# Performance work log

Hardware: AMD Instinct MI355X
Metric: run time of the kernel (lower is better)

## Reference

```python
import jax, jax.numpy as jnp
import numpy as np

N = 100000   # total nodes across all graphs
E = 200000   # directed edges
B = 128      # number of graphs in the batch
IN1, IN2 = 128, 128
IN = IN1 + IN2      # in_feats = 256 (x || x_da)
HID = 64
OUT = 64


def setup_inputs() -> dict:
    key = jax.random.key(0)
    ks = jax.random.split(key, 6)
    x = jax.random.normal(ks[0], (N, IN1), jnp.float32)
    x_da = jax.random.normal(ks[1], (N, IN2), jnp.float32)
    edge_index = jax.random.randint(ks[2], (2, E), 0, N, dtype=jnp.int32)
    # equal, sorted, non-empty segments (graph ids) -- mirrors sorted PyG batch vector
    batch = (jnp.arange(N, dtype=jnp.int32) * B) // N
    # root node of graph b = first node of its segment
    rootindex = (jnp.arange(B, dtype=jnp.int32) * N) // B
    s1 = 1.0 / np.sqrt(IN)
    W1 = jax.random.uniform(ks[3], (IN, HID), jnp.float32, -s1, s1)
    b1 = jnp.zeros((HID,), jnp.float32)
    s2 = 1.0 / np.sqrt(HID + IN)
    W2 = jax.random.uniform(ks[4], (HID + IN, OUT), jnp.float32, -s2, s2)
    b2 = jnp.zeros((OUT,), jnp.float32)
    return dict(x=x, x_da=x_da, edge_index=edge_index, batch=batch,
                rootindex=rootindex, W1=W1, b1=b1, W2=W2, b2=b2)


def gcn_conv(x, edge_index, W, b):
    """PyG GCNConv: symmetric-normalized A+I message passing after a linear."""
    n = x.shape[0]
    h = x @ W                                   # [n, out] linear first (as in PyG)
    src, dst = edge_index[0], edge_index[1]
    # degree on target nodes, +1 for the added self loop
    deg = jnp.zeros((n,), h.dtype).at[dst].add(jnp.ones((src.shape[0],), h.dtype)) + 1.0
    dinv = jax.lax.rsqrt(deg)
    norm = dinv[src] * dinv[dst]                # [E]
    agg = jnp.zeros_like(h).at[dst].add(h[src] * norm[:, None])
    agg = agg + h * (dinv * dinv)[:, None]      # self-loop term: 1/deg
    return agg + b


def reference(x, x_da, edge_index, batch, rootindex, W1, b1, W2, b2):
    x0 = jnp.concatenate([x, x_da], axis=1)     # [N, IN]
    x1 = x0                                     # saved original features
    h = gcn_conv(x0, edge_index, W1, b1)        # [N, HID]
    x2 = h                                      # saved conv1 output
    # vectorized root-feature broadcast: replaces the python per-graph loop
    root1 = x1[rootindex[batch]]                # [N, IN]
    h = jax.nn.relu(jnp.concatenate([h, root1], axis=1))  # [N, HID+IN]
    # F.dropout with training=False is identity (eval mode)
    h = gcn_conv(h, edge_index, W2, b2)         # [N, OUT]
    h = jax.nn.relu(h)
    root2 = x2[rootindex[batch]]                # [N, HID]
    h = jnp.concatenate([h, root2], axis=1)     # [N, OUT+HID]
    # scatter_mean over graph ids
    sums = jax.ops.segment_sum(h, batch, num_segments=B)
    counts = jax.ops.segment_sum(jnp.ones((h.shape[0], 1), h.dtype), batch, num_segments=B)
    return sums / counts                        # [B, OUT+HID]
```

## Files before the change

### kernel.cpp

```cpp
#include <hip/hip_runtime.h>

#define IN1 128
#define K1 256
#define HID 64
#define MCH 16

typedef __attribute__((ext_vector_type(8))) __bf16 bf16x8;
typedef __attribute__((ext_vector_type(4))) __bf16 bf16x4;
typedef __attribute__((ext_vector_type(8))) unsigned short u16x8;
typedef __attribute__((ext_vector_type(4))) float f32x4;

__device__ __forceinline__ int swz(int row, int k, int ldk) {
    return (row * ldk + k) ^ ((row & 7) << 3);
}

__global__ __launch_bounds__(256) void count_edges(const int* __restrict__ ei, int* counts, int E) {
    int e = blockIdx.x * 256 + threadIdx.x;
    if (e < E) atomicAdd(&counts[ei[E + e]], 1);
}

__global__ __launch_bounds__(256) void block_sums_dinv(const int* __restrict__ counts,
                                                       int* __restrict__ bsum,
                                                       float* __restrict__ dinv, int N) {
    __shared__ int sh[256];
    int i = blockIdx.x * 256 + threadIdx.x;
    int v = (i < N) ? counts[i] : 0;
    if (i < N) dinv[i] = rsqrtf((float)v + 1.0f);
    sh[threadIdx.x] = v;
    __syncthreads();
    for (int off = 128; off > 0; off >>= 1) {
        if (threadIdx.x < off) sh[threadIdx.x] += sh[threadIdx.x + off];
        __syncthreads();
    }
    if (threadIdx.x == 0) bsum[blockIdx.x] = sh[0];
}

__global__ __launch_bounds__(512) void scan_and_segs(const int* __restrict__ bsum,
                                                     int* __restrict__ boff, int nb,
                                                     const int* __restrict__ batch,
                                                     int* __restrict__ segs, int N, int B) {
    if (blockIdx.x == 0) {
        __shared__ int sh[512];
        int t = threadIdx.x;
        int v = (t < nb) ? bsum[t] : 0;
        sh[t] = v;
        __syncthreads();
        for (int off = 1; off < 512; off <<= 1) {
            int u = (t >= off) ? sh[t - off] : 0;
            __syncthreads();
            sh[t] += u;
            __syncthreads();
        }
        if (t < nb) boff[t] = sh[t] - v;
    } else {
        int b = threadIdx.x;
        if (b > B) return;
        if (b == B) { segs[B] = N; return; }
        int lo = 0, hi = N;
        while (lo < hi) {
            int mid = (lo + hi) >> 1;
            if (batch[mid] < b) lo = mid + 1; else hi = mid;
        }
        segs[b] = lo;
    }
}

__global__ __launch_bounds__(256) void write_rowstart(const int* __restrict__ counts,
                                                      const int* __restrict__ boff,
                                                      int* __restrict__ rowstart, int N, int E) {
    __shared__ int sh[256];
    int i = blockIdx.x * 256 + threadIdx.x;
    int t = threadIdx.x;
    int v = (i < N) ? counts[i] : 0;
    sh[t] = v;
    __syncthreads();
    for (int off = 1; off < 256; off <<= 1) {
        int u = (t >= off) ? sh[t - off] : 0;
        __syncthreads();
        sh[t] += u;
        __syncthreads();
    }
    if (i < N) rowstart[i] = boff[blockIdx.x] + sh[t] - v;
    if (i == 0) rowstart[N] = E;
}

__global__ __launch_bounds__(256) void scatter_csr(const int* __restrict__ ei,
                                                   const int* __restrict__ rowstart,
                                                   const float* __restrict__ dinv,
                                                   int* counts,
                                                   int* __restrict__ csr_src,
                                                   float* __restrict__ csr_w, int E) {
    int e = blockIdx.x * 256 + threadIdx.x;
    if (e >= E) return;
    int s = ei[e], d = ei[E + e];
    int pos = rowstart[d] + atomicSub(&counts[d], 1) - 1;
    csr_src[pos] = s;
    csr_w[pos] = dinv[s];
}

__global__ __launch_bounds__(256) void prep_w(const float* __restrict__ W1,
                                              const float* __restrict__ W2,
                                              __bf16* __restrict__ w1img,
                                              __bf16* __restrict__ w2img) {
    int tid = blockIdx.x * 256 + threadIdx.x;
    if (tid < 64 * K1) {
        int k = tid >> 6, n = tid & 63;
        w1img[swz(n, k, K1)] = (__bf16)W1[tid];
    } else if (tid < 64 * K1 + 64 * 64) {
        int e = tid - 64 * K1;
        int k = e >> 6, n = e & 63;
        w2img[swz(n, k, 64)] = (__bf16)W2[e];
    }
}

__global__ __launch_bounds__(256, 4) void gemm1_mfma(const float* __restrict__ x,
                                                     const float* __restrict__ xda,
                                                     const __bf16* __restrict__ w1img,
                                                     __bf16* __restrict__ h1, int N) {
    __shared__ __bf16 Ws[64 * K1];
    int tid = threadIdx.x;
#pragma unroll
    for (int i = 0; i < 8; ++i)
        reinterpret_cast<bf16x8*>(Ws)[i * 256 + tid] =
            reinterpret_cast<const bf16x8*>(w1img)[i * 256 + tid];
    __syncthreads();

    int w = tid >> 6, l = tid & 63;
    int lr = l & 15, lg = l >> 4;
    int arow = blockIdx.x * 64 + w * 16 + lr;
    int carow = min(arow, N - 1);
    const float4* px = reinterpret_cast<const float4*>(x + (size_t)carow * IN1) + lg * 2;
    const float4* pd = reinterpret_cast<const float4*>(xda + (size_t)carow * IN1) + lg * 2;

    f32x4 acc[4] = {};
    float4 buf[4][2];

#pragma unroll
    for (int t = 0; t < 4; ++t) {
        const float4* p = (t < 4) ? (px + t * 8) : (pd + (t - 4) * 8);
        buf[t][0] = p[0];
        buf[t][1] = p[1];
    }
#pragma unroll
    for (int t = 0; t < 8; ++t) {
        float4 fa = buf[t & 3][0], fb = buf[t & 3][1];
        if (t + 4 < 8) {
            int tn = t + 4;
            const float4* p = (tn < 4) ? (px + tn * 8) : (pd + (tn - 4) * 8);
            buf[t & 3][0] = p[0];
            buf[t & 3][1] = p[1];
        }
        bf16x8 af;
        af[0] = (__bf16)fa.x; af[1] = (__bf16)fa.y;
        af[2] = (__bf16)fa.z; af[3] = (__bf16)fa.w;
        af[4] = (__bf16)fb.x; af[5] = (__bf16)fb.y;
        af[6] = (__bf16)fb.z; af[7] = (__bf16)fb.w;
        int k0 = t * 32 + lg * 8;
#pragma unroll
        for (int c = 0; c < 4; ++c) {
            bf16x8 bfr = *reinterpret_cast<const bf16x8*>(&Ws[swz(c * 16 + lr, k0, K1)]);
            acc[c] = __builtin_amdgcn_mfma_f32_16x16x32_bf16(af, bfr, acc[c], 0, 0, 0);
        }
    }
#pragma unroll
    for (int c = 0; c < 4; ++c)
#pragma unroll
        for (int r = 0; r < 4; ++r) {
            int row = blockIdx.x * 64 + w * 16 + lg * 4 + r;
            if (row < N) h1[(size_t)row * HID + c * 16 + lr] = (__bf16)acc[c][r];
        }
}

__global__ __launch_bounds__(256, 4) void gemm2_mfma(const __bf16* __restrict__ x2,
                                                     const __bf16* __restrict__ w2img,
                                                     const float* __restrict__ rb2,
                                                     const int* __restrict__ batch,
                                                     __bf16* __restrict__ h2, int N) {
    __shared__ __bf16 Ws[64 * 64];
    int tid = threadIdx.x;
#pragma unroll
    for (int i = 0; i < 2; ++i)
        reinterpret_cast<bf16x8*>(Ws)[i * 256 + tid] =
            reinterpret_cast<const bf16x8*>(w2img)[i * 256 + tid];
    __syncthreads();

    int w = tid >> 6, l = tid & 63;
    int lr = l & 15, lg = l >> 4;
    int arow = blockIdx.x * 64 + w * 16 + lr;
    int carow = min(arow, N - 1);
    const u16x8* pa = reinterpret_cast<const u16x8*>(x2 + (size_t)carow * HID + lg * 8);

    u16x8 raw0 = pa[0];
    u16x8 raw1 = pa[2];
    f32x4 acc[4] = {};
#pragma unroll
    for (int t = 0; t < 2; ++t) {
        u16x8 raw = t ? raw1 : raw0;
        u16x8 rel;
#pragma unroll
        for (int i = 0; i < 8; ++i)
            rel[i] = (raw[i] & 0x8000) ? (unsigned short)0 : raw[i];
        bf16x8 af = *reinterpret_cast<bf16x8*>(&rel);
        int k0 = t * 32 + lg * 8;
#pragma unroll
        for (int c = 0; c < 4; ++c) {
            bf16x8 bfr = *reinterpret_cast<const bf16x8*>(&Ws[swz(c * 16 + lr, k0, 64)]);
            acc[c] = __builtin_amdgcn_mfma_f32_16x16x32_bf16(af, bfr, acc[c], 0, 0, 0);
        }
    }
#pragma unroll
    for (int r = 0; r < 4; ++r) {
        int row = blockIdx.x * 64 + w * 16 + lg * 4 + r;
        if (row >= N) continue;
        int b = batch[row];
        const float* rv = rb2 + (size_t)b * HID;
#pragma unroll
        for (int c = 0; c < 4; ++c)
            h2[(size_t)row * HID + c * 16 + lr] = (__bf16)(acc[c][r] + rv[c * 16 + lr]);
    }
}

__global__ __launch_bounds__(256) void gather(const int* __restrict__ rowstart,
                                              const int* __restrict__ csr_src,
                                              const float* __restrict__ csr_w,
                                              const __bf16* __restrict__ h,
                                              const float* __restrict__ dinv,
                                              const float* __restrict__ bias,
                                              __bf16* __restrict__ out, int N) {
    int t = blockIdx.x * 256 + threadIdx.x;
    int i = t >> 4, c = t & 15;
    if (i >= N) return;
    float di = dinv[i];
    float s2 = di * di;
    bf16x4 hv = *reinterpret_cast<const bf16x4*>(h + (size_t)i * HID + c * 4);
    float4 bv = reinterpret_cast<const float4*>(bias)[c];
    float a0 = fmaf((float)hv[0], s2, bv.x);
    float a1 = fmaf((float)hv[1], s2, bv.y);
    float a2 = fmaf((float)hv[2], s2, bv.z);
    float a3 = fmaf((float)hv[3], s2, bv.w);
    int k0 = rowstart[i], k1 = rowstart[i + 1];
    for (int k = k0; k < k1; ++k) {
        int s = csr_src[k];
        float wgt = csr_w[k] * di;
        bf16x4 sv = *reinterpret_cast<const bf16x4*>(h + (size_t)s * HID + c * 4);
        a0 = fmaf((float)sv[0], wgt, a0);
        a1 = fmaf((float)sv[1], wgt, a1);
        a2 = fmaf((float)sv[2], wgt, a2);
        a3 = fmaf((float)sv[3], wgt, a3);
    }
    bf16x4 o;
    o[0] = (__bf16)a0; o[1] = (__bf16)a1; o[2] = (__bf16)a2; o[3] = (__bf16)a3;
    *reinterpret_cast<bf16x4*>(out + (size_t)i * HID + c * 4) = o;
}

__global__ __launch_bounds__(64) void rb2_k(const float* __restrict__ x,
                                            const float* __restrict__ xda,
                                            const int* __restrict__ rootindex,
                                            const float* __restrict__ W2,
                                            float* __restrict__ rb2) {
    int b = blockIdx.x;
    int j = threadIdx.x;
    int root = rootindex[b];
    const float* xr = x + (size_t)root * IN1;
    const float* dr = xda + (size_t)root * IN1;
    float acc = 0.f;
    for (int k = 0; k < IN1; ++k) {
        float v = fmaxf(xr[k], 0.f);
        acc = fmaf(v, W2[(size_t)(HID + k) * HID + j], acc);
    }
    for (int k = 0; k < IN1; ++k) {
        float v = fmaxf(dr[k], 0.f);
        acc = fmaf(v, W2[(size_t)(HID + IN1 + k) * HID + j], acc);
    }
    rb2[b * HID + j] = acc;
}

__global__ __launch_bounds__(256) void mean_part(const __bf16* __restrict__ agg2,
                                                 const int* __restrict__ segs,
                                                 float* __restrict__ part) {
    int b = blockIdx.x / MCH, c = blockIdx.x % MCH;
    int s = segs[b], e = segs[b + 1];
    long len = e - s;
    int cs = s + (int)(len * c / MCH);
    int ce = s + (int)(len * (c + 1) / MCH);
    int f = threadIdx.x & 63, g = threadIdx.x >> 6;
    float p = 0.f;
    for (int i = cs + g; i < ce; i += 4)
        p += fmaxf((float)agg2[(size_t)i * HID + f], 0.f);
    __shared__ float red[4][64];
    red[g][f] = p;
    __syncthreads();
    if (g == 0)
        part[((size_t)b * MCH + c) * 64 + f] = red[0][f] + red[1][f] + red[2][f] + red[3][f];
}

__global__ __launch_bounds__(128) void mean_fin(const float* __restrict__ part,
                                                const __bf16* __restrict__ x2,
                                                const int* __restrict__ segs,
                                                const int* __restrict__ rootindex,
                                                float* __restrict__ out) {
    int b = blockIdx.x;
    int f = threadIdx.x;
    if (f < 64) {
        float s = 0.f;
#pragma unroll
        for (int c = 0; c < MCH; ++c) s += part[((size_t)b * MCH + c) * 64 + f];
        out[b * 128 + f] = s / (float)(segs[b + 1] - segs[b]);
    } else {
        int root = rootindex[b];
        out[b * 128 + f] = (float)x2[(size_t)root * HID + (f - 64)];
    }
}

extern "C" void kernel_launch(void* const* d_in, const int* in_sizes, int n_in,
                              void* d_out, int out_size, void* d_ws, size_t ws_size,
                              hipStream_t stream) {
    const float* x    = (const float*)d_in[0];
    const float* xda  = (const float*)d_in[1];
    const int*   ei   = (const int*)d_in[2];
    const int*   batch= (const int*)d_in[3];
    const int*   root = (const int*)d_in[4];
    const float* W1   = (const float*)d_in[5];
    const float* b1   = (const float*)d_in[6];
    const float* W2   = (const float*)d_in[7];
    const float* b2   = (const float*)d_in[8];
    float* out = (float*)d_out;

    int N = in_sizes[3];
    int E = in_sizes[2] / 2;
    int B = in_sizes[4];

    int gN   = (N + 255) / 256;
    int gE   = (E + 255) / 256;
    int gN16 = (N * 16 + 255) / 256;
    int gM   = (N + 63) / 64;
    int nb   = gN;

    auto align = [](size_t v) { return (v + 255) & ~(size_t)255; };
    char* w = (char*)d_ws;
    float* dinv   = (float*)w;  w += align((size_t)N * 4);
    int*   counts = (int*)w;    w += align((size_t)N * 4);
    int*   rowst  = (int*)w;    w += align((size_t)(N + 1) * 4);
    int*   bsum   = (int*)w;    w += align((size_t)nb * 4);
    int*   boff   = (int*)w;    w += align((size_t)nb * 4);
    int*   csr_src= (int*)w;    w += align((size_t)E * 4);
    float* csr_w  = (float*)w;  w += align((size_t)E * 4);
    __bf16* bufA  = (__bf16*)w; w += align((size_t)N * HID * 2);
    __bf16* bufB  = (__bf16*)w; w += align((size_t)N * HID * 2);
    __bf16* bufC  = (__bf16*)w; w += align((size_t)N * HID * 2);
    float* rb2    = (float*)w;  w += align((size_t)B * HID * 4);
    int*   segs   = (int*)w;    w += align((size_t)(B + 1) * 4);
    __bf16* w1img = (__bf16*)w; w += align((size_t)64 * K1 * 2);
    __bf16* w2img = (__bf16*)w; w += align((size_t)64 * 64 * 2);
    float* part   = (float*)w;  w += align((size_t)B * MCH * 64 * 4);

    hipMemsetAsync(counts, 0, (size_t)N * 4, stream);
    count_edges<<<gE, 256, 0, stream>>>(ei, counts, E);
    block_sums_dinv<<<gN, 256, 0, stream>>>(counts, bsum, dinv, N);
    scan_and_segs<<<2, 512, 0, stream>>>(bsum, boff, nb, batch, segs, N, B);
    write_rowstart<<<gN, 256, 0, stream>>>(counts, boff, rowst, N, E);
    scatter_csr<<<gE, 256, 0, stream>>>(ei, rowst, dinv, counts, csr_src, csr_w, E);
    prep_w<<<(64 * K1 + 64 * 64 + 255) / 256, 256, 0, stream>>>(W1, W2, w1img, w2img);
    rb2_k<<<B, 64, 0, stream>>>(x, xda, root, W2, rb2);

    gemm1_mfma<<<gM, 256, 0, stream>>>(x, xda, w1img, bufA, N);
    gather<<<gN16, 256, 0, stream>>>(rowst, csr_src, csr_w, bufA, dinv, b1, bufB, N);

    gemm2_mfma<<<gM, 256, 0, stream>>>(bufB, w2img, rb2, batch, bufA, N);
    gather<<<gN16, 256, 0, stream>>>(rowst, csr_src, csr_w, bufA, dinv, b2, bufC, N);

    mean_part<<<B * MCH, 256, 0, stream>>>(bufC, segs, part);
    mean_fin<<<B, 128, 0, stream>>>(part, bufB, segs, root, out);
}
```

Measured before the change: 239.5 us.

## Fuse gather with GEMM2 and gather with mean reduction; merge prep kernels

Fuses the first neighbour aggregation with the ReLU and the second MFMA GEMM in a 1024-thread block, keeping the aggregated tile in shared memory instead of writing and re-reading an intermediate buffer. Root rows of x2 are captured via binary search on rootindex. Fuses the second aggregation with ReLU and a per-block segmented reduction that adds into per-graph sums with atomics, replacing the two-stage mean kernels. It also merges weight prep with the root-bias kernel and zeroes counts and part with one memset. The cost is more shared-memory reduction barriers, float atomics that make the summation order nondeterministic, and larger blocks that may lower occupancy.

```diff
diff --git a/kernel.cpp b/kernel.cpp
--- a/kernel.cpp
+++ b/kernel.cpp
@@ -3,11 +3,9 @@
 #define IN1 128
 #define K1 256
 #define HID 64
-#define MCH 16
 
 typedef __attribute__((ext_vector_type(8))) __bf16 bf16x8;
 typedef __attribute__((ext_vector_type(4))) __bf16 bf16x4;
-typedef __attribute__((ext_vector_type(8))) unsigned short u16x8;
 typedef __attribute__((ext_vector_type(4))) float f32x4;
 
 __device__ __forceinline__ int swz(int row, int k, int ldk) {
@@ -98,18 +96,42 @@
     csr_w[pos] = dinv[s];
 }
 
-__global__ __launch_bounds__(256) void prep_w(const float* __restrict__ W1,
-                                              const float* __restrict__ W2,
-                                              __bf16* __restrict__ w1img,
-                                              __bf16* __restrict__ w2img) {
-    int tid = blockIdx.x * 256 + threadIdx.x;
-    if (tid < 64 * K1) {
-        int k = tid >> 6, n = tid & 63;
-        w1img[swz(n, k, K1)] = (__bf16)W1[tid];
-    } else if (tid < 64 * K1 + 64 * 64) {
-        int e = tid - 64 * K1;
-        int k = e >> 6, n = e & 63;
-        w2img[swz(n, k, 64)] = (__bf16)W2[e];
+__global__ __launch_bounds__(256) void prep_fused(const float* __restrict__ W1,
+                                                  const float* __restrict__ W2,
+                                                  __bf16* __restrict__ w1img,
+                                                  __bf16* __restrict__ w2img,
+                                                  const float* __restrict__ x,
+                                                  const float* __restrict__ xda,
+                                                  const int* __restrict__ rootindex,
+                                                  float* __restrict__ rb2) {
+    int blk = blockIdx.x;
+    if (blk < 80) {
+        int tid = blk * 256 + threadIdx.x;
+        if (tid < 64 * K1) {
+            int k = tid >> 6, n = tid & 63;
+            w1img[swz(n, k, K1)] = (__bf16)W1[tid];
+        } else if (tid < 64 * K1 + 64 * 64) {
+            int e = tid - 64 * K1;
+            int k = e >> 6, n = e & 63;
+            w2img[swz(n, k, 64)] = (__bf16)W2[e];
+        }
+    } else {
+        int b = blk - 80;
+        int root = rootindex[b];
+        int j = threadIdx.x & 63, q = threadIdx.x >> 6;
+        const float* xr = x + (size_t)root * IN1;
+        const float* dr = xda + (size_t)root * IN1;
+        float acc = 0.f;
+        for (int kk = 0; kk < 64; ++kk) {
+            int k = q * 64 + kk;
+            float v = (k < IN1) ? xr[k] : dr[k - IN1];
+            v = fmaxf(v, 0.f);
+            acc = fmaf(v, W2[(size_t)(HID + k) * HID + j], acc);
+        }
+        __shared__ float sh[4][64];
+        sh[q][j] = acc;
+        __syncthreads();
+        if (q == 0) rb2[b * HID + j] = sh[0][j] + sh[1][j] + sh[2][j] + sh[3][j];
     }
 }
 
@@ -137,7 +159,7 @@
 
 #pragma unroll
     for (int t = 0; t < 4; ++t) {
-        const float4* p = (t < 4) ? (px + t * 8) : (pd + (t - 4) * 8);
+        const float4* p = px + t * 8;
         buf[t][0] = p[0];
         buf[t][1] = p[1];
     }
@@ -146,7 +168,7 @@
         float4 fa = buf[t & 3][0], fb = buf[t & 3][1];
         if (t + 4 < 8) {
             int tn = t + 4;
-            const float4* p = (tn < 4) ? (px + tn * 8) : (pd + (tn - 4) * 8);
+            const float4* p = pd + (tn - 4) * 8;
             buf[t & 3][0] = p[0];
             buf[t & 3][1] = p[1];
         }
@@ -171,145 +193,167 @@
         }
 }
 
-__global__ __launch_bounds__(256, 4) void gemm2_mfma(const __bf16* __restrict__ x2,
-                                                     const __bf16* __restrict__ w2img,
-                                                     const float* __restrict__ rb2,
-                                                     const int* __restrict__ batch,
-                                                     __bf16* __restrict__ h2, int N) {
+__global__ __launch_bounds__(1024, 4) void conv2_fused(const int* __restrict__ rowstart,
+                                                       const int* __restrict__ csr_src,
+                                                       const float* __restrict__ csr_w,
+                                                       const __bf16* __restrict__ h1,
+                                                       const float* __restrict__ dinv,
+                                                       const float* __restrict__ bias1,
+                                                       const __bf16* __restrict__ w2img,
+                                                       const float* __restrict__ rb2,
+                                                       const int* __restrict__ batch,
+                                                       const int* __restrict__ rootindex,
+                                                       __bf16* __restrict__ h2,
+                                                       float* __restrict__ rootx2, int N, int B) {
+    __shared__ __bf16 As[64 * 64];
     __shared__ __bf16 Ws[64 * 64];
     int tid = threadIdx.x;
-#pragma unroll
-    for (int i = 0; i < 2; ++i)
-        reinterpret_cast<bf16x8*>(Ws)[i * 256 + tid] =
-            reinterpret_cast<const bf16x8*>(w2img)[i * 256 + tid];
-    __syncthreads();
-
-    int w = tid >> 6, l = tid & 63;
-    int lr = l & 15, lg = l >> 4;
-    int arow = blockIdx.x * 64 + w * 16 + lr;
-    int carow = min(arow, N - 1);
-    const u16x8* pa = reinterpret_cast<const u16x8*>(x2 + (size_t)carow * HID + lg * 8);
-
-    u16x8 raw0 = pa[0];
-    u16x8 raw1 = pa[2];
-    f32x4 acc[4] = {};
-#pragma unroll
-    for (int t = 0; t < 2; ++t) {
-        u16x8 raw = t ? raw1 : raw0;
-        u16x8 rel;
-#pragma unroll
-        for (int i = 0; i < 8; ++i)
-            rel[i] = (raw[i] & 0x8000) ? (unsigned short)0 : raw[i];
-        bf16x8 af = *reinterpret_cast<bf16x8*>(&rel);
-        int k0 = t * 32 + lg * 8;
-#pragma unroll
-        for (int c = 0; c < 4; ++c) {
-            bf16x8 bfr = *reinterpret_cast<const bf16x8*>(&Ws[swz(c * 16 + lr, k0, 64)]);
-            acc[c] = __builtin_amdgcn_mfma_f32_16x16x32_bf16(af, bfr, acc[c], 0, 0, 0);
-        }
-    }
-#pragma unroll
-    for (int r = 0; r < 4; ++r) {
-        int row = blockIdx.x * 64 + w * 16 + lg * 4 + r;
-        if (row >= N) continue;
-        int b = batch[row];
-        const float* rv = rb2 + (size_t)b * HID;
-#pragma unroll
-        for (int c = 0; c < 4; ++c)
-            h2[(size_t)row * HID + c * 16 + lr] = (__bf16)(acc[c][r] + rv[c * 16 + lr]);
-    }
-}
-
-__global__ __launch_bounds__(256) void gather(const int* __restrict__ rowstart,
-                                              const int* __restrict__ csr_src,
-                                              const float* __restrict__ csr_w,
-                                              const __bf16* __restrict__ h,
-                                              const float* __restrict__ dinv,
-                                              const float* __restrict__ bias,
-                                              __bf16* __restrict__ out, int N) {
-    int t = blockIdx.x * 256 + threadIdx.x;
-    int i = t >> 4, c = t & 15;
-    if (i >= N) return;
-    float di = dinv[i];
+    if (tid < 512)
+        reinterpret_cast<bf16x8*>(Ws)[tid] = reinterpret_cast<const bf16x8*>(w2img)[tid];
+
+    int nb0 = blockIdx.x * 64;
+    int ln = tid >> 4, cq = tid & 15;
+    int i = nb0 + ln;
+    bool ok = i < N;
+    int ci = ok ? i : N - 1;
+    float di = dinv[ci];
     float s2 = di * di;
-    bf16x4 hv = *reinterpret_cast<const bf16x4*>(h + (size_t)i * HID + c * 4);
-    float4 bv = reinterpret_cast<const float4*>(bias)[c];
+    bf16x4 hv = *reinterpret_cast<const bf16x4*>(h1 + (size_t)ci * HID + cq * 4);
+    float4 bv = reinterpret_cast<const float4*>(bias1)[cq];
     float a0 = fmaf((float)hv[0], s2, bv.x);
     float a1 = fmaf((float)hv[1], s2, bv.y);
     float a2 = fmaf((float)hv[2], s2, bv.z);
     float a3 = fmaf((float)hv[3], s2, bv.w);
-    int k0 = rowstart[i], k1 = rowstart[i + 1];
+    int k0 = rowstart[ci], k1 = rowstart[ci + 1];
     for (int k = k0; k < k1; ++k) {
         int s = csr_src[k];
         float wgt = csr_w[k] * di;
-        bf16x4 sv = *reinterpret_cast<const bf16x4*>(h + (size_t)s * HID + c * 4);
+        bf16x4 sv = *reinterpret_cast<const bf16x4*>(h1 + (size_t)s * HID + cq * 4);
         a0 = fmaf((float)sv[0], wgt, a0);
         a1 = fmaf((float)sv[1], wgt, a1);
         a2 = fmaf((float)sv[2], wgt, a2);
         a3 = fmaf((float)sv[3], wgt, a3);
     }
-    bf16x4 o;
-    o[0] = (__bf16)a0; o[1] = (__bf16)a1; o[2] = (__bf16)a2; o[3] = (__bf16)a3;
-    *reinterpret_cast<bf16x4*>(out + (size_t)i * HID + c * 4) = o;
-}
-
-__global__ __launch_bounds__(64) void rb2_k(const float* __restrict__ x,
-                                            const float* __restrict__ xda,
-                                            const int* __restrict__ rootindex,
-                                            const float* __restrict__ W2,
-                                            float* __restrict__ rb2) {
-    int b = blockIdx.x;
-    int j = threadIdx.x;
-    int root = rootindex[b];
-    const float* xr = x + (size_t)root * IN1;
-    const float* dr = xda + (size_t)root * IN1;
-    float acc = 0.f;
-    for (int k = 0; k < IN1; ++k) {
-        float v = fmaxf(xr[k], 0.f);
-        acc = fmaf(v, W2[(size_t)(HID + k) * HID + j], acc);
-    }
-    for (int k = 0; k < IN1; ++k) {
-        float v = fmaxf(dr[k], 0.f);
-        acc = fmaf(v, W2[(size_t)(HID + IN1 + k) * HID + j], acc);
-    }
-    rb2[b * HID + j] = acc;
-}
-
-__global__ __launch_bounds__(256) void mean_part(const __bf16* __restrict__ agg2,
-                                                 const int* __restrict__ segs,
-                                                 float* __restrict__ part) {
-    int b = blockIdx.x / MCH, c = blockIdx.x % MCH;
-    int s = segs[b], e = segs[b + 1];
-    long len = e - s;
-    int cs = s + (int)(len * c / MCH);
-    int ce = s + (int)(len * (c + 1) / MCH);
-    int f = threadIdx.x & 63, g = threadIdx.x >> 6;
-    float p = 0.f;
-    for (int i = cs + g; i < ce; i += 4)
-        p += fmaxf((float)agg2[(size_t)i * HID + f], 0.f);
-    __shared__ float red[4][64];
-    red[g][f] = p;
+    if (ok) {
+        int lo = 0, hi = B - 1, bfound = -1;
+        while (lo <= hi) {
+            int mid = (lo + hi) >> 1;
+            int rv = rootindex[mid];
+            if (rv == i) { bfound = mid; break; }
+            if (rv < i) lo = mid + 1; else hi = mid - 1;
+        }
+        if (bfound >= 0) {
+            float4 o = make_float4(a0, a1, a2, a3);
+            reinterpret_cast<float4*>(rootx2 + (size_t)bfound * 64)[cq] = o;
+        }
+    }
+    bf16x4 rl;
+    rl[0] = (__bf16)fmaxf(a0, 0.f); rl[1] = (__bf16)fmaxf(a1, 0.f);
+    rl[2] = (__bf16)fmaxf(a2, 0.f); rl[3] = (__bf16)fmaxf(a3, 0.f);
+    *reinterpret_cast<bf16x4*>(&As[swz(ln, cq * 4, 64)]) = rl;
     __syncthreads();
-    if (g == 0)
-        part[((size_t)b * MCH + c) * 64 + f] = red[0][f] + red[1][f] + red[2][f] + red[3][f];
+
+    int w = tid >> 6;
+    int rg = w >> 2, cb = w & 3;
+    int l = tid & 63, lr = l & 15, lg = l >> 4;
+    f32x4 acc = {};
+#pragma unroll
+    for (int t = 0; t < 2; ++t) {
+        int kk = t * 32 + lg * 8;
+        bf16x8 af = *reinterpret_cast<const bf16x8*>(&As[swz(rg * 16 + lr, kk, 64)]);
+        bf16x8 bfr = *reinterpret_cast<const bf16x8*>(&Ws[swz(cb * 16 + lr, kk, 64)]);
+        acc = __builtin_amdgcn_mfma_f32_16x16x32_bf16(af, bfr, acc, 0, 0, 0);
+    }
+#pragma unroll
+    for (int r = 0; r < 4; ++r) {
+        int row = nb0 + rg * 16 + lg * 4 + r;
+        if (row >= N) continue;
+        int b = batch[row];
+        h2[(size_t)row * HID + cb * 16 + lr] =
+            (__bf16)(acc[r] + rb2[(size_t)b * HID + cb * 16 + lr]);
+    }
+}
+
+__global__ __launch_bounds__(1024, 4) void conv3_mean(const int* __restrict__ rowstart,
+                                                      const int* __restrict__ csr_src,
+                                                      const float* __restrict__ csr_w,
+                                                      const __bf16* __restrict__ h2,
+                                                      const float* __restrict__ dinv,
+                                                      const float* __restrict__ bias2,
+                                                      const int* __restrict__ batch,
+                                                      float* __restrict__ part, int N) {
+    __shared__ float red[64][64];
+    int tid = threadIdx.x;
+    int nb0 = blockIdx.x * 64;
+    int ln = tid >> 4, cq = tid & 15;
+    int i = nb0 + ln;
+    bool ok = i < N;
+    int ci = ok ? i : N - 1;
+    float di = dinv[ci];
+    float s2 = di * di;
+    bf16x4 hv = *reinterpret_cast<const bf16x4*>(h2 + (size_t)ci * HID + cq * 4);
+    float4 bv = reinterpret_cast<const float4*>(bias2)[cq];
+    float a0 = fmaf((float)hv[0], s2, bv.x);
+    float a1 = fmaf((float)hv[1], s2, bv.y);
+    float a2 = fmaf((float)hv[2], s2, bv.z);
+    float a3 = fmaf((float)hv[3], s2, bv.w);
+    int k0 = rowstart[ci], k1 = rowstart[ci + 1];
+    for (int k = k0; k < k1; ++k) {
+        int s = csr_src[k];
+        float wgt = csr_w[k] * di;
+        bf16x4 sv = *reinterpret_cast<const bf16x4*>(h2 + (size_t)s * HID + cq * 4);
+        a0 = fmaf((float)sv[0], wgt, a0);
+        a1 = fmaf((float)sv[1], wgt, a1);
+        a2 = fmaf((float)sv[2], wgt, a2);
+        a3 = fmaf((float)sv[3], wgt, a3);
+    }
+    float v0 = fmaxf(a0, 0.f), v1 = fmaxf(a1, 0.f);
+    float v2 = fmaxf(a2, 0.f), v3 = fmaxf(a3, 0.f);
+
+    int gme = ok ? batch[i] : -1;
+    int g0 = batch[nb0];
+    int gLast = batch[min(nb0 + 63, N - 1)];
+    int g = g0;
+    while (true) {
+        float m = (gme == g) ? 1.f : 0.f;
+        int f = cq * 4;
+        red[ln][f + 0] = v0 * m;
+        red[ln][f + 1] = v1 * m;
+        red[ln][f + 2] = v2 * m;
+        red[ln][f + 3] = v3 * m;
+        __syncthreads();
+#pragma unroll
+        for (int off = 32; off > 0; off >>= 1) {
+            if (ln < off) {
+                red[ln][f + 0] += red[ln + off][f + 0];
+                red[ln][f + 1] += red[ln + off][f + 1];
+                red[ln][f + 2] += red[ln + off][f + 2];
+                red[ln][f + 3] += red[ln + off][f + 3];
+            }
+            __syncthreads();
+        }
+        if (ln == 0) {
+            atomicAdd(&part[(size_t)g * 64 + f + 0], red[0][f + 0]);
+            atomicAdd(&part[(size_t)g * 64 + f + 1], red[0][f + 1]);
+            atomicAdd(&part[(size_t)g * 64 + f + 2], red[0][f + 2]);
+            atomicAdd(&part[(size_t)g * 64 + f + 3], red[0][f + 3]);
+        }
+        if (g == gLast) break;
+        g = gLast;
+        __syncthreads();
+    }
 }
 
 __global__ __launch_bounds__(128) void mean_fin(const float* __restrict__ part,
-                                                const __bf16* __restrict__ x2,
+                                                const float* __restrict__ rootx2,
                                                 const int* __restrict__ segs,
-                                                const int* __restrict__ rootindex,
                                                 float* __restrict__ out) {
     int b = blockIdx.x;
     int f = threadIdx.x;
-    if (f < 64) {
-        float s = 0.f;
-#pragma unroll
-        for (int c = 0; c < MCH; ++c) s += part[((size_t)b * MCH + c) * 64 + f];
-        out[b * 128 + f] = s / (float)(segs[b + 1] - segs[b]);
-    } else {
-        int root = rootindex[b];
-        out[b * 128 + f] = (float)x2[(size_t)root * HID + (f - 64)];
-    }
+    if (f < 64)
+        out[b * 128 + f] = part[(size_t)b * 64 + f] / (float)(segs[b + 1] - segs[b]);
+    else
+        out[b * 128 + f] = rootx2[(size_t)b * 64 + (f - 64)];
 }
 
 extern "C" void kernel_launch(void* const* d_in, const int* in_sizes, int n_in,
@@ -330,45 +374,45 @@
     int E = in_sizes[2] / 2;
     int B = in_sizes[4];
 
-    int gN   = (N + 255) / 256;
-    int gE   = (E + 255) / 256;
-    int gN16 = (N * 16 + 255) / 256;
-    int gM   = (N + 63) / 64;
-    int nb   = gN;
+    int gN  = (N + 255) / 256;
+    int gE  = (E + 255) / 256;
+    int gM  = (N + 63) / 64;
+    int nb  = gN;
 
     auto align = [](size_t v) { return (v + 255) & ~(size_t)255; };
     char* w = (char*)d_ws;
+    int*   counts = (int*)w;    w += align((size_t)N * 4);
+    float* part   = (float*)w;  w += align((size_t)B * 64 * 4);
+    size_t zspan  = (char*)w - (char*)counts;
     float* dinv   = (float*)w;  w += align((size_t)N * 4);
-    int*   counts = (int*)w;    w += align((size_t)N * 4);
     int*   rowst  = (int*)w;    w += align((size_t)(N + 1) * 4);
     int*   bsum   = (int*)w;    w += align((size_t)nb * 4);
     int*   boff   = (int*)w;    w += align((size_t)nb * 4);
     int*   csr_src= (int*)w;    w += align((size_t)E * 4);
     float* csr_w  = (float*)w;  w += align((size_t)E * 4);
     __bf16* bufA  = (__bf16*)w; w += align((size_t)N * HID * 2);
-    __bf16* bufB  = (__bf16*)w; w += align((size_t)N * HID * 2);
     __bf16* bufC  = (__bf16*)w; w += align((size_t)N * HID * 2);
+    float* rootx2 = (float*)w;  w += align((size_t)B * 64 * 4);
     float* rb2    = (float*)w;  w += align((size_t)B * HID * 4);
     int*   segs   = (int*)w;    w += align((size_t)(B + 1) * 4);
     __bf16* w1img = (__bf16*)w; w += align((size_t)64 * K1 * 2);
     __bf16* w2img = (__bf16*)w; w += align((size_t)64 * 64 * 2);
-    float* part   = (float*)w;  w += align((size_t)B * MCH * 64 * 4);
-
-    hipMemsetAsync(counts, 0, (size_t)N * 4, stream);
+
+    hipMemsetAsync(counts, 0, zspan, stream);
     count_edges<<<gE, 256, 0, stream>>>(ei, counts, E);
     block_sums_dinv<<<gN, 256, 0, stream>>>(counts, bsum, dinv, N);
     scan_and_segs<<<2, 512, 0, stream>>>(bsum, boff, nb, batch, segs, N, B);
     write_rowstart<<<gN, 256, 0, stream>>>(counts, boff, rowst, N, E);
     scatter_csr<<<gE, 256, 0, stream>>>(ei, rowst, dinv, counts, csr_src, csr_w, E);
-    prep_w<<<(64 * K1 + 64 * 64 + 255) / 256, 256, 0, stream>>>(W1, W2, w1img, w2img);
-    rb2_k<<<B, 64, 0, stream>>>(x, xda, root, W2, rb2);
+    prep_fused<<<80 + B, 256, 0, stream>>>(W1, W2, w1img, w2img, x, xda, root, rb2);
 
     gemm1_mfma<<<gM, 256, 0, stream>>>(x, xda, w1img, bufA, N);
-    gather<<<gN16, 256, 0, stream>>>(rowst, csr_src, csr_w, bufA, dinv, b1, bufB, N);
-
-    gemm2_mfma<<<gM, 256, 0, stream>>>(bufB, w2img, rb2, batch, bufA, N);
-    gather<<<gN16, 256, 0, stream>>>(rowst, csr_src, csr_w, bufA, dinv, b2, bufC, N);
-
-    mean_part<<<B * MCH, 256, 0, stream>>>(bufC, segs, part);
-    mean_fin<<<B, 128, 0, stream>>>(part, bufB, segs, root, out);
-}
+
+    conv2_fused<<<gM, 1024, 0, stream>>>(rowst, csr_src, csr_w, bufA, dinv, b1,
+                                         w2img, rb2, batch, root, bufC, rootx2, N, B);
+
+    conv3_mean<<<gM, 1024, 0, stream>>>(rowst, csr_src, csr_w, bufC, dinv, b2,
+                                        batch, part, N);
+
+    mean_fin<<<B, 128, 0, stream>>>(part, rootx2, segs, out);
+}
```

After: 235.9 us. No clear change (-1.5%).
